# Kernel optimization log

Hardware: AMD Instinct MI355X
Metric: run time of the kernel (lower is better)

Reference implementation:

```python
import jax, jax.numpy as jnp
import numpy as np

N_NODES = 100000


def setup_inputs() -> dict:
    key = jax.random.key(0)
    k1, k2, k3 = jax.random.split(key, 3)
    x = jax.random.normal(k1, (N_NODES, 256), dtype=jnp.float32)
    edge_index = jax.random.randint(k2, (2, 1600000), 0, N_NODES, dtype=jnp.int64)
    # GCNConv learned params (glorot weight, zero bias as in PyG init)
    W = jax.random.normal(k3, (256, 64), dtype=jnp.float32) * (1.0 / np.sqrt(256.0))
    b = jnp.zeros((64,), dtype=jnp.float32)
    return {"x": x, "edge_index": edge_index, "W": W, "b": b}


def reference(x, edge_index, W, b):
    n = x.shape[0]
    # --- gcn_norm: add self-loops, symmetric normalization ---
    loops = jnp.arange(n, dtype=edge_index.dtype)
    row = jnp.concatenate([edge_index[0], loops])  # source nodes
    col = jnp.concatenate([edge_index[1], loops])  # target nodes
    ones = jnp.ones(row.shape[0], dtype=x.dtype)
    deg = jax.ops.segment_sum(ones, col, num_segments=n)  # [N]
    dinv = jnp.where(deg > 0, jax.lax.rsqrt(deg), 0.0)
    norm = dinv[row] * dinv[col]  # [E+N]
    # --- linear transform then normalized scatter-add aggregation ---
    h = x @ W  # [N, out]
    msgs = h[row] * norm[:, None]  # [E+N, out]
    out = jax.ops.segment_sum(msgs, col, num_segments=n)  # [N, out]
    return out + b
```

## Files before the change

kernel.cpp:

```cpp
#include <hip/hip_runtime.h>


#define IN_F 256
#define OUT_F 64
#define WBITS 9
#define MAXBINS 256
#define CSHIFT 23
#define ROWMASK 0x7FFFFFu
#define SCAT_BLOCKS 512

typedef unsigned short ushort_t;
typedef short bf16x8 __attribute__((ext_vector_type(8)));
typedef float f32x4 __attribute__((ext_vector_type(4)));

static __device__ __forceinline__ unsigned f2bf1(float f) {
    unsigned u = __float_as_uint(f);
    return (u + 0x7FFFu + ((u >> 16) & 1u)) >> 16;
}
static __device__ __forceinline__ unsigned pk2(float a, float b) {
    return f2bf1(a) | (f2bf1(b) << 16);
}
static __device__ __forceinline__ ushort_t f2bf(float f) { return (ushort_t)f2bf1(f); }
static __device__ __forceinline__ float bf2f(ushort_t h) {
    return __uint_as_float(((unsigned)h) << 16);
}

__global__ __launch_bounds__(256) void init_kernel(const float* __restrict__ W,
                                                   ushort_t* __restrict__ wfrag,
                                                   const int* __restrict__ col,
                                                   int* __restrict__ binCnt,
                                                   int* __restrict__ partialCnt,
                                                   int E, int nbins) {
    int gt = blockIdx.x * 256 + threadIdx.x;
    if (gt < 2048) {
        int t = gt;
        int kk = t >> 8;
        int ct = (t >> 6) & 3;
        int l  = t & 63;
        int k0 = kk * 32 + (l >> 4) * 8;
        int c  = ct * 16 + (l & 15);
        unsigned u0 = pk2(W[(k0 + 0) * OUT_F + c], W[(k0 + 1) * OUT_F + c]);
        unsigned u1 = pk2(W[(k0 + 2) * OUT_F + c], W[(k0 + 3) * OUT_F + c]);
        unsigned u2 = pk2(W[(k0 + 4) * OUT_F + c], W[(k0 + 5) * OUT_F + c]);
        unsigned u3 = pk2(W[(k0 + 6) * OUT_F + c], W[(k0 + 7) * OUT_F + c]);
        ((uint4*)wfrag)[t] = make_uint4(u0, u1, u2, u3);
    }
    __shared__ int hist[MAXBINS];
    int tid = threadIdx.x;
    if (tid < nbins) hist[tid] = 0;
    __syncthreads();
    int chunk = (E + SCAT_BLOCKS - 1) / SCAT_BLOCKS;
    int s = blockIdx.x * chunk;
    int epos = min(E, s + chunk);
    for (int e = s + tid; e < epos; e += 256)
        atomicAdd(&hist[col[e] >> WBITS], 1);
    __syncthreads();
    if (tid < nbins) {
        int c = hist[tid];
        partialCnt[blockIdx.x * MAXBINS + tid] = c;
        if (c) atomicAdd(&binCnt[tid], c);
    }
}

__global__ void bin_scan_kernel(const int* __restrict__ binCnt, int* __restrict__ binStart,
                                int* __restrict__ binCursor, int* __restrict__ start_n,
                                int nbins) {
    __shared__ int lds[MAXBINS];
    int tid = threadIdx.x;
    int v = (tid < nbins) ? binCnt[tid] : 0;
    lds[tid] = v;
    __syncthreads();
    for (int d = 1; d < MAXBINS; d <<= 1) {
        int t = (tid >= d) ? lds[tid - d] : 0;
        __syncthreads();
        lds[tid] += t;
        __syncthreads();
    }
    if (tid < nbins) {
        int ex = lds[tid] - v;
        binStart[tid] = ex;
        binCursor[tid] = ex;
    }
    if (tid == MAXBINS - 1) {
        binStart[nbins] = lds[MAXBINS - 1];
        start_n[0] = lds[MAXBINS - 1];
    }
}

__global__ __launch_bounds__(256) void mega_kernel(const float* __restrict__ x,
                                                   const ushort_t* __restrict__ wfrag,
                                                   ushort_t* __restrict__ h,
                                                   const int* __restrict__ row,
                                                   const int* __restrict__ col,
                                                   const int* __restrict__ partialCnt,
                                                   int* __restrict__ binCursor,
                                                   unsigned* __restrict__ ebuf,
                                                   int n, int E, int nbins, int gemmBlocks) {
    __shared__ int cur[MAXBINS];
    int tid = threadIdx.x;

    if (blockIdx.x < gemmBlocks) {
        int l  = tid & 63;
        int lr = l & 15;
        int lg = l >> 4;
        int rowbase = blockIdx.x * 64 + (tid >> 6) * 16;
        int arow = rowbase + lr;
        int lrow = (arow < n) ? arow : (n - 1);
        const float* xp = x + (size_t)lrow * IN_F + lg * 8;
        const uint4* wf = (const uint4*)wfrag;

        f32x4 acc0 = {0.f, 0.f, 0.f, 0.f};
        f32x4 acc1 = {0.f, 0.f, 0.f, 0.f};
        f32x4 acc2 = {0.f, 0.f, 0.f, 0.f};
        f32x4 acc3 = {0.f, 0.f, 0.f, 0.f};

        #pragma unroll
        for (int kk = 0; kk < 8; ++kk) {
            float4 xa = *(const float4*)(xp + kk * 32);
            float4 xb = *(const float4*)(xp + kk * 32 + 4);
            union { bf16x8 v; unsigned u[4]; } A;
            A.u[0] = pk2(xa.x, xa.y);
            A.u[1] = pk2(xa.z, xa.w);
            A.u[2] = pk2(xb.x, xb.y);
            A.u[3] = pk2(xb.z, xb.w);
            union { uint4 q; bf16x8 v; } B0, B1, B2, B3;
            B0.q = wf[(kk * 4 + 0) * 64 + l];
            B1.q = wf[(kk * 4 + 1) * 64 + l];
            B2.q = wf[(kk * 4 + 2) * 64 + l];
            B3.q = wf[(kk * 4 + 3) * 64 + l];
            acc0 = __builtin_amdgcn_mfma_f32_16x16x32_bf16(A.v, B0.v, acc0, 0, 0, 0);
            acc1 = __builtin_amdgcn_mfma_f32_16x16x32_bf16(A.v, B1.v, acc1, 0, 0, 0);
            acc2 = __builtin_amdgcn_mfma_f32_16x16x32_bf16(A.v, B2.v, acc2, 0, 0, 0);
            acc3 = __builtin_amdgcn_mfma_f32_16x16x32_bf16(A.v, B3.v, acc3, 0, 0, 0);
        }

        #pragma unroll
        for (int q = 0; q < 4; ++q) {
            int r = rowbase + lg * 4 + q;
            if (r < n) {
                ushort_t* gp = h + (size_t)r * OUT_F + lr;
                gp[0]  = f2bf(acc0[q]);
                gp[16] = f2bf(acc1[q]);
                gp[32] = f2bf(acc2[q]);
                gp[48] = f2bf(acc3[q]);
            }
        }
    } else {
        int sb = blockIdx.x - gemmBlocks;
        if (tid < nbins) {
            int c = partialCnt[sb * MAXBINS + tid];
            cur[tid] = c ? atomicAdd(&binCursor[tid], c) : 0;
        }
        __syncthreads();
        int chunk = (E + SCAT_BLOCKS - 1) / SCAT_BLOCKS;
        int s = sb * chunk;
        int epos = min(E, s + chunk);
        for (int e = s + tid; e < epos; e += 256) {
            int cc = col[e];
            int pos = atomicAdd(&cur[cc >> WBITS], 1);
            ebuf[pos] = (unsigned)row[e] | ((unsigned)(cc & ((1 << WBITS) - 1)) << CSHIFT);
        }
    }
}

__global__ __launch_bounds__(512) void fine_build_kernel(const unsigned* __restrict__ ebuf,
                                                         const int* __restrict__ binStart,
                                                         int* __restrict__ start,
                                                         float* __restrict__ dinv,
                                                         int* __restrict__ bucket, int n) {
    __shared__ int sdeg[512];
    __shared__ int scur[512];
    int b = blockIdx.x;
    int lo = b << WBITS;
    int wcnt = min(512, n - lo);
    int tid = threadIdx.x;
    sdeg[tid] = 0;
    __syncthreads();
    int s = binStart[b], epos = binStart[b + 1];
    for (int e = s + tid; e < epos; e += 512)
        atomicAdd(&sdeg[ebuf[e] >> CSHIFT], 1);
    __syncthreads();
    int d = sdeg[tid];
    if (tid < wcnt) dinv[lo + tid] = rsqrtf((float)(d + 1));
    for (int dd = 1; dd < 512; dd <<= 1) {
        int t = (tid >= dd) ? sdeg[tid - dd] : 0;
        __syncthreads();
        sdeg[tid] += t;
        __syncthreads();
    }
    int ex = sdeg[tid] - d;
    if (tid < wcnt) start[lo + tid] = s + ex;
    scur[tid] = ex;
    __syncthreads();
    for (int e = s + tid; e < epos; e += 512) {
        unsigned pr = ebuf[e];
        int pos = atomicAdd(&scur[pr >> CSHIFT], 1);
        bucket[s + pos] = (int)(pr & ROWMASK);
    }
}

__global__ __launch_bounds__(256) void gather_kernel(const int* __restrict__ start,
                              const int* __restrict__ bucket, const ushort_t* __restrict__ h,
                              const float* __restrict__ dinv, const float* __restrict__ b,
                              float* __restrict__ out, int n) {
    int lane = threadIdx.x & 63;
    int node = blockIdx.x * 4 + (threadIdx.x >> 6);
    if (node >= n) return;
    int f8  = lane & 7;
    int grp = lane >> 3;
    int s0  = start[node];
    int cnt = start[node + 1] - s0;
    const int* bp = bucket + s0;
    int last = cnt - 1;

    float a0 = 0.f, a1 = 0.f, a2 = 0.f, a3 = 0.f;
    float a4 = 0.f, a5 = 0.f, a6 = 0.f, a7 = 0.f;
    union { uint4 q; ushort_t s[8]; } VA, VB;
    for (int e0 = 0; e0 < cnt; e0 += 16) {
        int eA = e0 + grp;
        int eB = e0 + 8 + grp;
        int iA = bp[min(eA, last)];
        int iB = bp[min(eB, last)];
        VA.q = *(const uint4*)(h + (size_t)iA * OUT_F + f8 * 8);
        VB.q = *(const uint4*)(h + (size_t)iB * OUT_F + f8 * 8);
        float dA = (eA < cnt) ? dinv[iA] : 0.f;
        float dB = (eB < cnt) ? dinv[iB] : 0.f;
        a0 += bf2f(VA.s[0]) * dA;
        a1 += bf2f(VA.s[1]) * dA;
        a2 += bf2f(VA.s[2]) * dA;
        a3 += bf2f(VA.s[3]) * dA;
        a4 += bf2f(VA.s[4]) * dA;
        a5 += bf2f(VA.s[5]) * dA;
        a6 += bf2f(VA.s[6]) * dA;
        a7 += bf2f(VA.s[7]) * dA;
        a0 += bf2f(VB.s[0]) * dB;
        a1 += bf2f(VB.s[1]) * dB;
        a2 += bf2f(VB.s[2]) * dB;
        a3 += bf2f(VB.s[3]) * dB;
        a4 += bf2f(VB.s[4]) * dB;
        a5 += bf2f(VB.s[5]) * dB;
        a6 += bf2f(VB.s[6]) * dB;
        a7 += bf2f(VB.s[7]) * dB;
    }
    #pragma unroll
    for (int off = 8; off < 64; off <<= 1) {
        a0 += __shfl_xor(a0, off, 64);
        a1 += __shfl_xor(a1, off, 64);
        a2 += __shfl_xor(a2, off, 64);
        a3 += __shfl_xor(a3, off, 64);
        a4 += __shfl_xor(a4, off, 64);
        a5 += __shfl_xor(a5, off, 64);
        a6 += __shfl_xor(a6, off, 64);
        a7 += __shfl_xor(a7, off, 64);
    }

    if (grp == 0) {
        union { uint4 q; ushort_t s[8]; } SV;
        SV.q = *(const uint4*)(h + (size_t)node * OUT_F + f8 * 8);
        float dc = dinv[node];
        const float4* bv = (const float4*)b;
        float4 o0, o1;
        o0.x = (a0 + bf2f(SV.s[0]) * dc) * dc + bv[f8 * 2].x;
        o0.y = (a1 + bf2f(SV.s[1]) * dc) * dc + bv[f8 * 2].y;
        o0.z = (a2 + bf2f(SV.s[2]) * dc) * dc + bv[f8 * 2].z;
        o0.w = (a3 + bf2f(SV.s[3]) * dc) * dc + bv[f8 * 2].w;
        o1.x = (a4 + bf2f(SV.s[4]) * dc) * dc + bv[f8 * 2 + 1].x;
        o1.y = (a5 + bf2f(SV.s[5]) * dc) * dc + bv[f8 * 2 + 1].y;
        o1.z = (a6 + bf2f(SV.s[6]) * dc) * dc + bv[f8 * 2 + 1].z;
        o1.w = (a7 + bf2f(SV.s[7]) * dc) * dc + bv[f8 * 2 + 1].w;
        float4* op = (float4*)(out + (size_t)node * OUT_F + f8 * 8);
        op[0] = o0;
        op[1] = o1;
    }
}

extern "C" void kernel_launch(void* const* d_in, const int* in_sizes, int n_in,
                              void* d_out, int out_size, void* d_ws, size_t ws_size,
                              hipStream_t stream) {
    const float* x  = (const float*)d_in[0];
    const int*   ei = (const int*)d_in[1];
    const float* W  = (const float*)d_in[2];
    const float* b  = (const float*)d_in[3];
    float* out = (float*)d_out;

    int n = in_sizes[0] / IN_F;
    int E = in_sizes[1] / 2;
    const int* rowp = ei;
    const int* colp = ei + E;

    int nbins = (n + (1 << WBITS) - 1) >> WBITS;

    char* wp = (char*)d_ws;
    ushort_t* h    = (ushort_t*)wp;
    unsigned* ebuf = (unsigned*)(wp + (size_t)n * OUT_F * 2);
    int* bucket    = (int*)(ebuf + E);
    ushort_t* wfrag = (ushort_t*)(bucket + E);
    int* start     = (int*)(wfrag + 16384);
    float* dinv    = (float*)(start + n + 1);
    int* binCnt    = (int*)(dinv + n);
    int* binStart  = binCnt + MAXBINS;
    int* binCursor = binStart + MAXBINS + 1;
    int* partialCnt= binCursor + MAXBINS;

    int gemmBlocks = (n + 63) / 64;

    hipMemsetAsync(binCnt, 0, MAXBINS * sizeof(int), stream);
    init_kernel<<<SCAT_BLOCKS, 256, 0, stream>>>(W, wfrag, colp, binCnt, partialCnt, E, nbins);
    bin_scan_kernel<<<1, MAXBINS, 0, stream>>>(binCnt, binStart, binCursor, start + n, nbins);
    mega_kernel<<<gemmBlocks + SCAT_BLOCKS, 256, 0, stream>>>(x, wfrag, h, rowp, colp,
                                                              partialCnt, binCursor, ebuf,
                                                              n, E, nbins, gemmBlocks);
    fine_build_kernel<<<nbins, 512, 0, stream>>>(ebuf, binStart, start, dinv, bucket, n);
    gather_kernel<<<(n + 3) / 4, 256, 0, stream>>>(start, bucket, h, dinv, b, out, n);
}
```

Before: 133.9 us.

## Locally sort scatter chunks in LDS before writing coarse bins to global

```diff
diff --git a/kernel.cpp b/kernel.cpp
--- a/kernel.cpp
+++ b/kernel.cpp
@@ -7,7 +7,7 @@
 #define MAXBINS 256
 #define CSHIFT 23
 #define ROWMASK 0x7FFFFFu
-#define SCAT_BLOCKS 512
+#define CHUNK 4096
 
 typedef unsigned short ushort_t;
 typedef short bf16x8 __attribute__((ext_vector_type(8)));
@@ -49,9 +49,8 @@
     int tid = threadIdx.x;
     if (tid < nbins) hist[tid] = 0;
     __syncthreads();
-    int chunk = (E + SCAT_BLOCKS - 1) / SCAT_BLOCKS;
-    int s = blockIdx.x * chunk;
-    int epos = min(E, s + chunk);
+    int s = blockIdx.x * CHUNK;
+    int epos = min(E, s + CHUNK);
     for (int e = s + tid; e < epos; e += 256)
         atomicAdd(&hist[col[e] >> WBITS], 1);
     __syncthreads();
@@ -96,7 +95,6 @@
                                                    int* __restrict__ binCursor,
                                                    unsigned* __restrict__ ebuf,
                                                    int n, int E, int nbins, int gemmBlocks) {
-    __shared__ int cur[MAXBINS];
     int tid = threadIdx.x;
 
     if (blockIdx.x < gemmBlocks) {
@@ -146,20 +144,43 @@
             }
         }
     } else {
+        __shared__ int gbase[MAXBINS];
+        __shared__ int lbase[MAXBINS];
+        __shared__ int lcur[MAXBINS];
+        __shared__ unsigned sorted[CHUNK];
+        __shared__ int sdst[CHUNK];
+
         int sb = blockIdx.x - gemmBlocks;
-        if (tid < nbins) {
-            int c = partialCnt[sb * MAXBINS + tid];
-            cur[tid] = c ? atomicAdd(&binCursor[tid], c) : 0;
+        int s = sb * CHUNK;
+        int epos = min(E, s + CHUNK);
+
+        int c = (tid < nbins) ? partialCnt[sb * MAXBINS + tid] : 0;
+        if (tid < nbins) gbase[tid] = c ? atomicAdd(&binCursor[tid], c) : 0;
+        lbase[tid] = c;
+        __syncthreads();
+        for (int d = 1; d < MAXBINS; d <<= 1) {
+            int t = (tid >= d) ? lbase[tid - d] : 0;
+            __syncthreads();
+            lbase[tid] += t;
+            __syncthreads();
         }
-        __syncthreads();
-        int chunk = (E + SCAT_BLOCKS - 1) / SCAT_BLOCKS;
-        int s = sb * chunk;
-        int epos = min(E, s + chunk);
+        int ex = lbase[tid] - c;
+        lbase[tid] = ex;
+        lcur[tid] = ex;
+        __syncthreads();
+
         for (int e = s + tid; e < epos; e += 256) {
             int cc = col[e];
-            int pos = atomicAdd(&cur[cc >> WBITS], 1);
-            ebuf[pos] = (unsigned)row[e] | ((unsigned)(cc & ((1 << WBITS) - 1)) << CSHIFT);
+            int bin = cc >> WBITS;
+            int slot = atomicAdd(&lcur[bin], 1);
+            sorted[slot] = (unsigned)row[e] | ((unsigned)(cc & ((1 << WBITS) - 1)) << CSHIFT);
+            sdst[slot]   = gbase[bin] + (slot - lbase[bin]);
         }
+        __syncthreads();
+
+        int csize = epos - s;
+        for (int i = tid; i < csize; i += 256)
+            ebuf[sdst[i]] = sorted[i];
     }
 }
 
@@ -289,6 +310,7 @@
     const int* colp = ei + E;
 
     int nbins = (n + (1 << WBITS) - 1) >> WBITS;
+    int SB = (E + CHUNK - 1) / CHUNK;
 
     char* wp = (char*)d_ws;
     ushort_t* h    = (ushort_t*)wp;
@@ -305,11 +327,11 @@
     int gemmBlocks = (n + 63) / 64;
 
     hipMemsetAsync(binCnt, 0, MAXBINS * sizeof(int), stream);
-    init_kernel<<<SCAT_BLOCKS, 256, 0, stream>>>(W, wfrag, colp, binCnt, partialCnt, E, nbins);
+    init_kernel<<<SB, 256, 0, stream>>>(W, wfrag, colp, binCnt, partialCnt, E, nbins);
     bin_scan_kernel<<<1, MAXBINS, 0, stream>>>(binCnt, binStart, binCursor, start + n, nbins);
-    mega_kernel<<<gemmBlocks + SCAT_BLOCKS, 256, 0, stream>>>(x, wfrag, h, rowp, colp,
-                                                              partialCnt, binCursor, ebuf,
-                                                              n, E, nbins, gemmBlocks);
+    mega_kernel<<<gemmBlocks + SB, 256, 0, stream>>>(x, wfrag, h, rowp, colp,
+                                                     partialCnt, binCursor, ebuf,
+                                                     n, E, nbins, gemmBlocks);
     fine_build_kernel<<<nbins, 512, 0, stream>>>(ebuf, binStart, start, dinv, bucket, n);
     gather_kernel<<<(n + 3) / 4, 256, 0, stream>>>(start, bucket, h, dinv, b, out, n);
 }
```

Result: faster. 127.8 us (median of 2 runs) (-4.5%).
